# Kernel optimization log

Hardware: AMD Instinct MI355X
Metric: run time of the kernel (lower is better)

Reference implementation:

```python
import jax, jax.numpy as jnp
import numpy as np

VOL = 100.0  # cubic volume (100,100,100)


def _forward(x, positions, input_weights, features, output_weights,
             connection_radii, thresholds, n_iterations):
    # clamp positions into the volume (per-axis, min 0.1, max VOL-0.1)
    pos = jnp.clip(positions, 0.1, VOL - 0.1)                      # [N,3]
    radii = jnp.clip(connection_radii, 1.0, 50.0)                  # [N]
    # pairwise Euclidean distances via ||a||^2 + ||b||^2 - 2ab (avoids [N,N,3])
    sq = jnp.sum(pos * pos, axis=1)
    d2 = jnp.maximum(sq[:, None] + sq[None, :] - 2.0 * (pos @ pos.T), 0.0)
    pos_mask = d2 > 0.0
    dist = jnp.where(pos_mask, jnp.sqrt(jnp.where(pos_mask, d2, 1.0)), 0.0)  # [N,N]
    max_r = jnp.max(radii)
    conn_mask = (dist < max_r).astype(dist.dtype)
    atten = jnp.exp(-jnp.minimum(dist / (radii[:, None] + 1e-6), 20.0)) * conn_mask
    # feature similarity (F.normalize uses eps as a clamp-min on the norm)
    fn = features / jnp.maximum(jnp.linalg.norm(features, axis=1, keepdims=True), 1e-6)
    feat_sim = fn @ fn.T                                            # [N,N]
    cw = atten * (0.3 + 0.7 * jnp.clip(feat_sim, -1.0, 1.0))
    cw = cw / (jnp.sum(cw, axis=1, keepdims=True) + 1e-6)           # row-normalized [N,N]
    # spatial input / output gating along x-axis
    xc = jnp.clip(pos[:, 0] / VOL, 0.0, 1.0)                        # [N]
    iw = jnp.exp(-3.0 * xc)
    iw = iw / (jnp.sum(iw) + 1e-6)
    act = (x @ input_weights.T) * iw                                # [B,N]
    for _ in range(n_iterations):
        act = jnp.minimum(jax.nn.relu(act + act @ cw.T - thresholds), 100.0)
    ow = jnp.exp(3.0 * (xc - 1.0))
    ow = ow / (jnp.sum(ow) + 1e-6)
    return (act * ow) @ output_weights                              # [B,out]


def setup_inputs() -> dict:
    key = jax.random.key(0)
    ks = jax.random.split(key, 5)
    N, IN, OUT, FD, B = 8000, 784, 10, 32, 64
    return {
        "x": jax.random.normal(ks[0], (B, IN), jnp.float32),
        "positions": jax.random.uniform(ks[1], (N, 3), jnp.float32) * VOL,
        "input_weights": jax.random.normal(ks[2], (N, IN), jnp.float32) * 0.01,
        "features": jax.random.normal(ks[3], (N, FD), jnp.float32) * 0.1,
        "output_weights": jax.random.normal(ks[4], (N, OUT), jnp.float32) * 0.01,
        "connection_radii": jnp.ones((N,), jnp.float32) * 15.0,
        "thresholds": jnp.zeros((N,), jnp.float32),
        "n_iterations": 2,
    }


def reference(x, positions, input_weights, features, output_weights,
              connection_radii, thresholds, n_iterations):
    return _forward(x, positions, input_weights, features, output_weights,
                    connection_radii, thresholds, n_iterations)
```

## Files before the change

### kernel.cpp

```cpp
#include <hip/hip_runtime.h>
#include <hip/hip_bf16.h>
#include <math.h>

#define VOLF 100.0f
#define FD 32
#define OUT_DIM 10
#define MAXN 320
#define MAX_LAUNCH_ITERS 4
#define KSPLIT 7
#define BM 64
#define BKQ 28
#define SRW 4
#define SRB 16
#define OB 128

__global__ __launch_bounds__(256) void k_pre(
    const float* __restrict__ positions, const float* __restrict__ radii_in,
    const float* __restrict__ features, float* __restrict__ posx4,
    float* __restrict__ radii, float* __restrict__ e_iw, float* __restrict__ e_ow,
    float* __restrict__ fn, float* __restrict__ scal, int N)
{
    int i = blockIdx.x * blockDim.x + threadIdx.x;
    float my_iw = 0.0f, my_ow = 0.0f, my_r = 0.0f;
    if (i < N) {
        float px = fminf(fmaxf(positions[3*i+0], 0.1f), VOLF - 0.1f);
        float py = fminf(fmaxf(positions[3*i+1], 0.1f), VOLF - 0.1f);
        float pz = fminf(fmaxf(positions[3*i+2], 0.1f), VOLF - 0.1f);
        float sq = px*px + py*py + pz*pz;
        posx4[4*i+0] = px; posx4[4*i+1] = py; posx4[4*i+2] = pz; posx4[4*i+3] = sq;
        float r = fminf(fmaxf(radii_in[i], 1.0f), 50.0f);
        radii[i] = r; my_r = r;
        float xc = fminf(fmaxf(px / VOLF, 0.0f), 1.0f);
        my_iw = expf(-3.0f * xc);
        my_ow = expf(3.0f * (xc - 1.0f));
        e_iw[i] = my_iw; e_ow[i] = my_ow;
        float s = 0.0f;
        #pragma unroll
        for (int k = 0; k < FD; k++) { float v = features[(size_t)i*FD + k]; s += v*v; }
        float nrm = fmaxf(sqrtf(s), 1e-6f);
        #pragma unroll
        for (int k = 0; k < FD; k++) fn[(size_t)i*FD + k] = features[(size_t)i*FD + k] / nrm;
    }
    __shared__ float red[256];
    red[threadIdx.x] = my_iw; __syncthreads();
    for (int s = 128; s > 0; s >>= 1) { if (threadIdx.x < s) red[threadIdx.x] += red[threadIdx.x + s]; __syncthreads(); }
    if (threadIdx.x == 0) atomicAdd(&scal[0], red[0]);
    __syncthreads();
    red[threadIdx.x] = my_ow; __syncthreads();
    for (int s = 128; s > 0; s >>= 1) { if (threadIdx.x < s) red[threadIdx.x] += red[threadIdx.x + s]; __syncthreads(); }
    if (threadIdx.x == 0) atomicAdd(&scal[1], red[0]);
    if (i < N) atomicMax((int*)&scal[2], __float_as_int(my_r));
}

__global__ __launch_bounds__(256) void k_xt(const float* __restrict__ x, float* __restrict__ xT,
                                            int B, int IN)
{
    int idx = blockIdx.x * blockDim.x + threadIdx.x;
    if (idx < B * IN) {
        int b = idx / IN, k = idx % IN;
        xT[(size_t)k * B + b] = x[idx];
    }
}

__global__ __launch_bounds__(256) void k_act0(
    const float* __restrict__ xT, const float* __restrict__ Wi,
    float* __restrict__ partial, int N, int IN)
{
    __shared__ float4 xs4[BKQ * 64];
    __shared__ float  wt[BM * 112];
    int t = threadIdx.x;
    int i0 = blockIdx.x * BM;
    int k0 = blockIdx.y * 112;
    #pragma unroll
    for (int fi = t; fi < BM * 28; fi += 256) {
        int row = fi / 28, cq = fi % 28;
        ((float4*)wt)[row * 28 + cq] = *(const float4*)(Wi + (size_t)(i0 + row) * IN + k0 + cq * 4);
    }
    {
        int l = t & 63, q = t >> 6;
        #pragma unroll
        for (int kq = q; kq < BKQ; kq += 4) {
            float4 v;
            v.x = xT[(size_t)(k0 + 4*kq + 0) * 64 + l];
            v.y = xT[(size_t)(k0 + 4*kq + 1) * 64 + l];
            v.z = xT[(size_t)(k0 + 4*kq + 2) * 64 + l];
            v.w = xT[(size_t)(k0 + 4*kq + 3) * 64 + l];
            xs4[kq * 64 + l] = v;
        }
    }
    __syncthreads();
    int wave = t >> 6, lane = t & 63;
    int nbase = wave * 16;
    float acc[16];
    #pragma unroll
    for (int n = 0; n < 16; n++) acc[n] = 0.0f;
    for (int kq = 0; kq < BKQ; kq++) {
        float4 xv = xs4[kq * 64 + lane];
        #pragma unroll
        for (int n = 0; n < 16; n++) {
            float4 w = ((const float4*)(wt + (nbase + n) * 112))[kq];
            acc[n] += w.x * xv.x + w.y * xv.y + w.z * xv.z + w.w * xv.w;
        }
    }
    size_t base = ((size_t)blockIdx.y * N + (i0 + nbase)) * 64 + lane;
    #pragma unroll
    for (int n = 0; n < 16; n++)
        partial[base + (size_t)n * 64] = acc[n];
}

__global__ __launch_bounds__(256) void k_act0_red(
    const float* __restrict__ partial, const float* __restrict__ e_iw,
    const float* __restrict__ scal, float* __restrict__ actA, int N)
{
    int idx = blockIdx.x * 256 + threadIdx.x;
    int i = idx >> 6;
    size_t stride = (size_t)N * 64;
    float s = 0.0f;
    #pragma unroll
    for (int ks = 0; ks < KSPLIT; ks++) s += partial[ks * stride + idx];
    float inv = 1.0f / (scal[0] + 1e-6f);
    actA[idx] = s * (e_iw[i] * inv);
}

__global__ __launch_bounds__(256) void k_scan(
    const float* __restrict__ posx4, const float* __restrict__ scal,
    int* __restrict__ nbr_idx, float* __restrict__ nbr_w ,
    int* __restrict__ nbr_cnt, int N)
{
    int wave = threadIdx.x >> 6, lane = threadIdx.x & 63;
    int r0 = blockIdx.x * SRB + wave * SRW;
    float4 pi[SRW];
    #pragma unroll
    for (int t = 0; t < SRW; t++) pi[t] = ((const float4*)posx4)[r0 + t];
    float maxr = __int_as_float(((const int*)scal)[2]);
    unsigned long long lmask = (1ull << lane) - 1ull;
    int cnt[SRW] = {0, 0, 0, 0};
    for (int jb = 0; jb < N; jb += 64) {
        int j = jb + lane;
        float4 pj = ((const float4*)posx4)[j];
        #pragma unroll
        for (int t = 0; t < SRW; t++) {
            float d2 = fmaxf(pi[t].w + pj.w - 2.0f*(pi[t].x*pj.x + pi[t].y*pj.y + pi[t].z*pj.z), 0.0f);
            float dist = sqrtf(d2);
            bool hit = dist < maxr;
            unsigned long long m = __ballot(hit);
            if (m) {
                if (hit) {
                    int pos = cnt[t] + __popcll(m & lmask);
                    if (pos < MAXN) {
                        nbr_idx[(size_t)(r0 + t) * MAXN + pos] = j;
                        nbr_w [(size_t)(r0 + t) * MAXN + pos] = dist;
                    }
                }
                cnt[t] += (int)__popcll(m);
            }
        }
    }
    if (lane == 0) {
        #pragma unroll
        for (int t = 0; t < SRW; t++)
            nbr_cnt[r0 + t] = min(cnt[t], MAXN);
    }
}

__global__ __launch_bounds__(256) void k_weight(
    const float* __restrict__ fn, const float* __restrict__ radii,
    const int* __restrict__ nbr_idx, float* __restrict__ nbr_w ,
    const int* __restrict__ nbr_cnt, float* __restrict__ rowinv, int N)
{
    int i = blockIdx.x;
    int lane = threadIdx.x & 63;
    int wave = threadIdx.x >> 6;
    int sub = lane & 7;
    int eg  = lane >> 3;
    float4 fni = ((const float4*)(fn + (size_t)i * FD))[sub];
    float inv_ri = 1.0f / (radii[i] + 1e-6f);
    int cnt = nbr_cnt[i];
    float s = 0.0f;
    for (int e0 = wave * 8; e0 < cnt; e0 += 32) {
        int e = e0 + eg;
        bool act = e < cnt;
        int ecl = act ? e : (cnt - 1);
        int j      = nbr_idx[(size_t)i * MAXN + ecl];
        float dist = nbr_w [(size_t)i * MAXN + ecl];
        float4 fj = ((const float4*)(fn + (size_t)j * FD))[sub];
        float fs = fni.x*fj.x + fni.y*fj.y + fni.z*fj.z + fni.w*fj.w;
        fs += __shfl_xor(fs, 1, 64);
        fs += __shfl_xor(fs, 2, 64);
        fs += __shfl_xor(fs, 4, 64);
        fs = fminf(fmaxf(fs, -1.0f), 1.0f);
        float w = expf(-fminf(dist * inv_ri, 20.0f)) * (0.3f + 0.7f * fs);
        if (act && sub == 0) {
            nbr_w[(size_t)i * MAXN + e] = w;
            s += w;
        }
    }
    __shared__ float red[256];
    red[threadIdx.x] = s; __syncthreads();
    for (int st = 128; st > 0; st >>= 1) { if (threadIdx.x < st) red[threadIdx.x] += red[threadIdx.x + st]; __syncthreads(); }
    if (threadIdx.x == 0) rowinv[i] = 1.0f / (red[0] + 1e-6f);
}

__global__ __launch_bounds__(256) void k_iter(
    const float* __restrict__ actIn, float* __restrict__ actOut,
    const int* __restrict__ nbr_idx, const float* __restrict__ nbr_w,
    const int* __restrict__ nbr_cnt, const float* __restrict__ rowinv,
    const float* __restrict__ thr,
    const int* __restrict__ nIterPtr, int iterIdx, int N)
{
    if (iterIdx >= min(*nIterPtr, MAX_LAUNCH_ITERS)) return;
    int i = blockIdx.x;
    int wave = threadIdx.x >> 6, lane = threadIdx.x & 63;
    int cnt = nbr_cnt[i];
    float acc = 0.0f;
    for (int e = wave; e < cnt; e += 4) {
        int j   = nbr_idx[(size_t)i * MAXN + e];
        float w = nbr_w [(size_t)i * MAXN + e];
        acc += actIn[(size_t)j * 64 + lane] * w;
    }
    __shared__ float redA[4 * 64];
    redA[wave * 64 + lane] = acc;
    __syncthreads();
    if (wave == 0) {
        float tot = redA[lane] + redA[64 + lane] + redA[128 + lane] + redA[192 + lane];
        float v = actIn[(size_t)i * 64 + lane] + tot * rowinv[i] - thr[i];
        v = fminf(fmaxf(v, 0.0f), 100.0f);
        actOut[(size_t)i * 64 + lane] = v;
    }
}

__global__ __launch_bounds__(256) void k_out1(
    const float* __restrict__ actA, const float* __restrict__ actB,
    const int* __restrict__ nIterPtr, const float* __restrict__ e_ow,
    const float* __restrict__ scal, const float* __restrict__ outW,
    float* __restrict__ outPart, int N)
{
    int m = min(*nIterPtr, MAX_LAUNCH_ITERS);
    const float* actF = (m & 1) ? actB : actA;
    int wave = threadIdx.x >> 6, lane = threadIdx.x & 63;
    float inv = 1.0f / (scal[1] + 1e-6f);
    float acc[OUT_DIM];
    #pragma unroll
    for (int o = 0; o < OUT_DIM; o++) acc[o] = 0.0f;
    for (int i = blockIdx.x * 4 + wave; i < N; i += OB * 4) {
        float a = actF[(size_t)i * 64 + lane] * (e_ow[i] * inv);
        const float* wo = outW + (size_t)i * OUT_DIM;
        #pragma unroll
        for (int o = 0; o < OUT_DIM; o++) acc[o] += a * wo[o];
    }
    __shared__ float red[4][OUT_DIM][64];
    #pragma unroll
    for (int o = 0; o < OUT_DIM; o++) red[wave][o][lane] = acc[o];
    __syncthreads();
    if (wave == 0) {
        #pragma unroll
        for (int o = 0; o < OUT_DIM; o++) {
            float s = red[0][o][lane] + red[1][o][lane] + red[2][o][lane] + red[3][o][lane];
            outPart[((size_t)blockIdx.x * OUT_DIM + o) * 64 + lane] = s;
        }
    }
}

__global__ __launch_bounds__(256) void k_out2(
    const float* __restrict__ outPart, float* __restrict__ out)
{
    int t = blockIdx.x * 256 + threadIdx.x;
    if (t >= 64 * OUT_DIM) return;
    int b = t / OUT_DIM, o = t % OUT_DIM;
    float s = 0.0f;
    for (int blk = 0; blk < OB; blk++)
        s += outPart[((size_t)blk * OUT_DIM + o) * 64 + b];
    out[t] = s;
}

extern "C" void kernel_launch(void* const* d_in, const int* in_sizes, int n_in,
                              void* d_out, int out_size, void* d_ws, size_t ws_size,
                              hipStream_t stream)
{
    const float* x        = (const float*)d_in[0];
    const float* positions= (const float*)d_in[1];
    const float* Win      = (const float*)d_in[2];
    const float* features = (const float*)d_in[3];
    const float* Wout     = (const float*)d_in[4];
    const float* radii_in = (const float*)d_in[5];
    const float* thr      = (const float*)d_in[6];
    const int*   nIter    = (const int*)  d_in[7];

    const int N  = in_sizes[5];
    const int IN = in_sizes[2] / N;
    const int B  = in_sizes[0] / IN;
    (void)B;

    float* ws = (float*)d_ws;
    size_t off = 0;
    auto alloc = [&](size_t nfloats) { size_t cur = off; off += (nfloats + 63) & ~(size_t)63; return cur; };
    float* xT      = ws + alloc((size_t)B * IN);
    float* posx4   = ws + alloc((size_t)N * 4);
    float* radii   = ws + alloc(N);
    float* e_iw    = ws + alloc(N);
    float* e_ow    = ws + alloc(N);
    float* rowinv  = ws + alloc(N);
    float* scal    = ws + alloc(4);
    float* outPart = ws + alloc((size_t)OB * OUT_DIM * 64);
    float* fn      = ws + alloc((size_t)N * FD);
    float* actA    = ws + alloc((size_t)N * 64);
    float* actB    = ws + alloc((size_t)N * 64);
    float* nbr_w   = ws + alloc((size_t)N * MAXN);
    int*   nbr_idx = (int*)(ws + alloc((size_t)N * MAXN));
    int*   nbr_cnt = (int*)(ws + alloc(N));
    float* partial = nbr_w;

    hipMemsetAsync(scal, 0, 4 * sizeof(float), stream);

    k_pre<<<(N + 255) / 256, 256, 0, stream>>>(positions, radii_in, features,
                                               posx4, radii, e_iw, e_ow, fn, scal, N);
    k_xt<<<(B * IN + 255) / 256, 256, 0, stream>>>(x, xT, B, IN);
    k_act0<<<dim3(N / BM, KSPLIT), 256, 0, stream>>>(xT, Win, partial, N, IN);
    k_act0_red<<<(N * 64) / 256, 256, 0, stream>>>(partial, e_iw, scal, actA, N);
    k_scan<<<N / SRB, 256, 0, stream>>>(posx4, scal, nbr_idx, nbr_w, nbr_cnt, N);
    k_weight<<<N, 256, 0, stream>>>(fn, radii, nbr_idx, nbr_w, nbr_cnt, rowinv, N);

    float* bufs[2] = {actA, actB};
    for (int it = 0; it < MAX_LAUNCH_ITERS; it++) {
        k_iter<<<N, 256, 0, stream>>>(bufs[it & 1], bufs[(it + 1) & 1],
                                      nbr_idx, nbr_w, nbr_cnt, rowinv, thr, nIter, it, N);
    }
    k_out1<<<OB, 256, 0, stream>>>(actA, actB, nIter, e_ow, scal, Wout, outPart, N);
    k_out2<<<3, 256, 0, stream>>>(outPart, (float*)d_out);
}
```

Before: 268.4 us.

## Interleave neighbor index and weight into int2 edges; rebalance scan rows

Result: faster. 254.4 us (-5.2%).

```diff
diff --git a/kernel.cpp b/kernel.cpp
--- a/kernel.cpp
+++ b/kernel.cpp
@@ -10,8 +10,8 @@
 #define KSPLIT 7
 #define BM 64
 #define BKQ 28
-#define SRW 4
-#define SRB 16
+#define SRW 2
+#define SRB 8
 #define OB 128
 
 __global__ __launch_bounds__(256) void k_pre(
@@ -122,50 +122,60 @@
     actA[idx] = s * (e_iw[i] * inv);
 }
 
+__device__ __forceinline__ void scan_body(
+    const float4& p, const float4& q, int j, float maxr,
+    unsigned long long lmask, int2* __restrict__ ep, size_t base, int& cnt)
+{
+    float d2 = fmaxf(p.w + q.w - 2.0f*(p.x*q.x + p.y*q.y + p.z*q.z), 0.0f);
+    float dist = sqrtf(d2);
+    bool hit = dist < maxr;
+    unsigned long long m = __ballot(hit);
+    if (m) {
+        if (hit) {
+            int pos = cnt + (int)__popcll(m & lmask);
+            if (pos < MAXN) ep[base + pos] = make_int2(j, __float_as_int(dist));
+        }
+        cnt += (int)__popcll(m);
+    }
+}
+
 __global__ __launch_bounds__(256) void k_scan(
     const float* __restrict__ posx4, const float* __restrict__ scal,
-    int* __restrict__ nbr_idx, float* __restrict__ nbr_w ,
-    int* __restrict__ nbr_cnt, int N)
+    int2* __restrict__ ep, int* __restrict__ nbr_cnt, int N)
 {
     int wave = threadIdx.x >> 6, lane = threadIdx.x & 63;
     int r0 = blockIdx.x * SRB + wave * SRW;
-    float4 pi[SRW];
-    #pragma unroll
-    for (int t = 0; t < SRW; t++) pi[t] = ((const float4*)posx4)[r0 + t];
+    float4 p0 = ((const float4*)posx4)[r0];
+    float4 p1 = ((const float4*)posx4)[r0 + 1];
     float maxr = __int_as_float(((const int*)scal)[2]);
     unsigned long long lmask = (1ull << lane) - 1ull;
-    int cnt[SRW] = {0, 0, 0, 0};
-    for (int jb = 0; jb < N; jb += 64) {
-        int j = jb + lane;
-        float4 pj = ((const float4*)posx4)[j];
-        #pragma unroll
-        for (int t = 0; t < SRW; t++) {
-            float d2 = fmaxf(pi[t].w + pj.w - 2.0f*(pi[t].x*pj.x + pi[t].y*pj.y + pi[t].z*pj.z), 0.0f);
-            float dist = sqrtf(d2);
-            bool hit = dist < maxr;
-            unsigned long long m = __ballot(hit);
-            if (m) {
-                if (hit) {
-                    int pos = cnt[t] + __popcll(m & lmask);
-                    if (pos < MAXN) {
-                        nbr_idx[(size_t)(r0 + t) * MAXN + pos] = j;
-                        nbr_w [(size_t)(r0 + t) * MAXN + pos] = dist;
-                    }
-                }
-                cnt[t] += (int)__popcll(m);
-            }
-        }
+    int c0 = 0, c1 = 0;
+    size_t base0 = (size_t)r0 * MAXN, base1 = base0 + MAXN;
+    int jb = 0;
+    for (; jb + 128 <= N; jb += 128) {
+        int j0 = jb + lane, j1 = jb + 64 + lane;
+        float4 q0 = ((const float4*)posx4)[j0];
+        float4 q1 = ((const float4*)posx4)[j1];
+        scan_body(p0, q0, j0, maxr, lmask, ep, base0, c0);
+        scan_body(p1, q0, j0, maxr, lmask, ep, base1, c1);
+        scan_body(p0, q1, j1, maxr, lmask, ep, base0, c0);
+        scan_body(p1, q1, j1, maxr, lmask, ep, base1, c1);
+    }
+    for (; jb < N; jb += 64) {
+        int j0 = jb + lane;
+        float4 q0 = ((const float4*)posx4)[j0];
+        scan_body(p0, q0, j0, maxr, lmask, ep, base0, c0);
+        scan_body(p1, q0, j0, maxr, lmask, ep, base1, c1);
     }
     if (lane == 0) {
-        #pragma unroll
-        for (int t = 0; t < SRW; t++)
-            nbr_cnt[r0 + t] = min(cnt[t], MAXN);
+        nbr_cnt[r0]     = min(c0, MAXN);
+        nbr_cnt[r0 + 1] = min(c1, MAXN);
     }
 }
 
 __global__ __launch_bounds__(256) void k_weight(
     const float* __restrict__ fn, const float* __restrict__ radii,
-    const int* __restrict__ nbr_idx, float* __restrict__ nbr_w ,
+    int2* __restrict__ ep ,
     const int* __restrict__ nbr_cnt, float* __restrict__ rowinv, int N)
 {
     int i = blockIdx.x;
@@ -181,8 +191,9 @@
         int e = e0 + eg;
         bool act = e < cnt;
         int ecl = act ? e : (cnt - 1);
-        int j      = nbr_idx[(size_t)i * MAXN + ecl];
-        float dist = nbr_w [(size_t)i * MAXN + ecl];
+        int2 edge = ep[(size_t)i * MAXN + ecl];
+        int j      = edge.x;
+        float dist = __int_as_float(edge.y);
         float4 fj = ((const float4*)(fn + (size_t)j * FD))[sub];
         float fs = fni.x*fj.x + fni.y*fj.y + fni.z*fj.z + fni.w*fj.w;
         fs += __shfl_xor(fs, 1, 64);
@@ -191,7 +202,7 @@
         fs = fminf(fmaxf(fs, -1.0f), 1.0f);
         float w = expf(-fminf(dist * inv_ri, 20.0f)) * (0.3f + 0.7f * fs);
         if (act && sub == 0) {
-            nbr_w[(size_t)i * MAXN + e] = w;
+            ((float*)&ep[(size_t)i * MAXN + e])[1] = w;
             s += w;
         }
     }
@@ -203,9 +214,8 @@
 
 __global__ __launch_bounds__(256) void k_iter(
     const float* __restrict__ actIn, float* __restrict__ actOut,
-    const int* __restrict__ nbr_idx, const float* __restrict__ nbr_w,
-    const int* __restrict__ nbr_cnt, const float* __restrict__ rowinv,
-    const float* __restrict__ thr,
+    const int2* __restrict__ ep, const int* __restrict__ nbr_cnt,
+    const float* __restrict__ rowinv, const float* __restrict__ thr,
     const int* __restrict__ nIterPtr, int iterIdx, int N)
 {
     if (iterIdx >= min(*nIterPtr, MAX_LAUNCH_ITERS)) return;
@@ -214,9 +224,8 @@
     int cnt = nbr_cnt[i];
     float acc = 0.0f;
     for (int e = wave; e < cnt; e += 4) {
-        int j   = nbr_idx[(size_t)i * MAXN + e];
-        float w = nbr_w [(size_t)i * MAXN + e];
-        acc += actIn[(size_t)j * 64 + lane] * w;
+        int2 edge = ep[(size_t)i * MAXN + e];
+        acc += actIn[(size_t)edge.x * 64 + lane] * __int_as_float(edge.y);
     }
     __shared__ float redA[4 * 64];
     redA[wave * 64 + lane] = acc;
@@ -305,10 +314,9 @@
     float* fn      = ws + alloc((size_t)N * FD);
     float* actA    = ws + alloc((size_t)N * 64);
     float* actB    = ws + alloc((size_t)N * 64);
-    float* nbr_w   = ws + alloc((size_t)N * MAXN);
-    int*   nbr_idx = (int*)(ws + alloc((size_t)N * MAXN));
+    int2*  ep      = (int2*)(ws + alloc((size_t)N * MAXN * 2));
     int*   nbr_cnt = (int*)(ws + alloc(N));
-    float* partial = nbr_w;
+    float* partial = (float*)ep;
 
     hipMemsetAsync(scal, 0, 4 * sizeof(float), stream);
 
@@ -317,13 +325,13 @@
     k_xt<<<(B * IN + 255) / 256, 256, 0, stream>>>(x, xT, B, IN);
     k_act0<<<dim3(N / BM, KSPLIT), 256, 0, stream>>>(xT, Win, partial, N, IN);
     k_act0_red<<<(N * 64) / 256, 256, 0, stream>>>(partial, e_iw, scal, actA, N);
-    k_scan<<<N / SRB, 256, 0, stream>>>(posx4, scal, nbr_idx, nbr_w, nbr_cnt, N);
-    k_weight<<<N, 256, 0, stream>>>(fn, radii, nbr_idx, nbr_w, nbr_cnt, rowinv, N);
+    k_scan<<<N / SRB, 256, 0, stream>>>(posx4, scal, ep, nbr_cnt, N);
+    k_weight<<<N, 256, 0, stream>>>(fn, radii, ep, nbr_cnt, rowinv, N);
 
     float* bufs[2] = {actA, actB};
     for (int it = 0; it < MAX_LAUNCH_ITERS; it++) {
         k_iter<<<N, 256, 0, stream>>>(bufs[it & 1], bufs[(it + 1) & 1],
-                                      nbr_idx, nbr_w, nbr_cnt, rowinv, thr, nIter, it, N);
+                                      ep, nbr_cnt, rowinv, thr, nIter, it, N);
     }
     k_out1<<<OB, 256, 0, stream>>>(actA, actB, nIter, e_ow, scal, Wout, outPart, N);
     k_out2<<<3, 256, 0, stream>>>(outPart, (float*)d_out);
```
